# Performance work log

Hardware: AMD Instinct MI355X
Metric: run time of the kernel (lower is better)

## Reference

```python
import jax, jax.numpy as jnp
import numpy as np

B, H, N, D = 1, 8, 2048, 64  # n >> d: fastmax's intended long-seq / small-head-dim regime


def setup_inputs() -> dict:
    key = jax.random.key(0)
    kq, kk, kv, kr = jax.random.split(key, 4)
    q = jax.random.normal(kq, (B, H, N, D), dtype=jnp.float32)
    k = jax.random.normal(kk, (B, H, N, D), dtype=jnp.float32)
    v = jax.random.normal(kv, (B, H, N, D), dtype=jnp.float32)
    rpe_matrix = jax.random.normal(kr, (2 * N - 1, D), dtype=jnp.float32)
    return {"q": q, "k": k, "v": v, "rpe_matrix": rpe_matrix, "mask": 1}


def reference(q, k, v, rpe_matrix, mask):
    # Fastmax: 2nd-order Taylor approximation of softmax attention,
    # weight(i,j) = 1 + s_ij + s_ij^2 / 2 where s_ij = q_i . (k_j) + q_i . rpe[i-j+n-1],
    # normalized by the row-sum, optionally causal (mask).
    b, h, n, d = q.shape
    # content scores: (b,h,n,n)
    s = jnp.einsum('bhid,bhjd->bhij', q, k)
    # RPE scores: project q onto every relative-position embedding, then gather
    # the (i,j) -> i-j+n-1 diagonal structure.  qr: (b,h,n,2n-1)
    qr = jnp.einsum('bhid,md->bhim', q, rpe_matrix)
    i = jnp.arange(n)[:, None]
    j = jnp.arange(n)[None, :]
    rel = i - j + (n - 1)  # (n,n) in [0, 2n-2]
    s = s + jnp.take_along_axis(qr, rel[None, None], axis=-1)
    # Taylor-2 exp approximation
    w = 1.0 + s + 0.5 * s * s
    if mask:  # causal
        w = jnp.where(j <= i, w, 0.0)
    denom = jnp.sum(w, axis=-1, keepdims=True)  # (b,h,n,1)
    out = jnp.einsum('bhij,bhjd->bhid', w, v) / denom
    return out
```

## Files before the change

kernel.cpp:

```cpp
#include <hip/hip_runtime.h>
#include <hip/hip_bf16.h>

#define HH 8
#define NN 2048
#define DD 64

typedef __attribute__((ext_vector_type(8))) short bf16x8;
typedef __attribute__((ext_vector_type(4))) float f32x4;
typedef __attribute__((ext_vector_type(8))) unsigned short u16x8;
typedef unsigned short ushort_t;

static __device__ __forceinline__ unsigned short f2bf(float x) {
    union { float f; unsigned u; } un; un.f = x;
    unsigned r = un.u + 0x7FFFu + ((un.u >> 16) & 1u);
    return (unsigned short)(r >> 16);
}
static __device__ __forceinline__ unsigned short f2bf_t(float x) {
    union { float f; unsigned u; } un; un.f = x;
    return (unsigned short)(un.u >> 16);
}
static __device__ __forceinline__ float bf2f(unsigned short u) {
    union { unsigned u; float f; } un; un.u = ((unsigned)u) << 16;
    return un.f;
}

#define OFF_Q  0u
#define OFF_K  2097152u
#define OFF_VT 4194304u
#define OFF_R  6291456u
#define OFF_P  6815744u
#define WS_NEED 11272192u

#define NQ4 262144
#define NR4 65520
#define CVT_BLOCKS 2305
__global__ void pre_kernel(const float* __restrict__ q, const float* __restrict__ k,
                           const float* __restrict__ r, const float* __restrict__ v,
                           ushort_t* __restrict__ ws) {
    __shared__ __align__(16) ushort_t T[64][72];
    if (blockIdx.x < CVT_BLOCKS) {
        int idx = blockIdx.x * 256 + threadIdx.x;
        const float* src; ushort_t* dst; int off;
        if (idx < NQ4) { src = q; dst = (ushort_t*)((char*)ws + OFF_Q); off = idx; }
        else if (idx < 2 * NQ4) { src = k; dst = (ushort_t*)((char*)ws + OFF_K); off = idx - NQ4; }
        else if (idx < 2 * NQ4 + NR4) { src = r; dst = (ushort_t*)((char*)ws + OFF_R); off = idx - 2 * NQ4; }
        else return;
        float4 f = *(const float4*)&src[4 * (size_t)off];
        ushort4 u; u.x = f2bf(f.x); u.y = f2bf(f.y); u.z = f2bf(f.z); u.w = f2bf(f.w);
        *(ushort4*)&dst[4 * (size_t)off] = u;
    } else {
        ushort_t* vt = (ushort_t*)((char*)ws + OFF_VT);
        const int bb = blockIdx.x - CVT_BLOCKS;
        const int h = bb >> 5;
        const int n0 = (bb & 31) * 64;
        const int tid = threadIdx.x;
        const float* vh = v + (size_t)h * NN * DD;
        #pragma unroll
        for (int p = 0; p < 4; ++p) {
            int c = tid + 256 * p; int rr = c >> 4, dc = (c & 15) << 2;
            float4 f = *(const float4*)&vh[(size_t)(n0 + rr) * DD + dc];
            T[dc + 0][rr] = f2bf(f.x); T[dc + 1][rr] = f2bf(f.y);
            T[dc + 2][rr] = f2bf(f.z); T[dc + 3][rr] = f2bf(f.w);
        }
        __syncthreads();
        #pragma unroll
        for (int p = 0; p < 2; ++p) {
            int c = tid + 256 * p; int d = c >> 3, nn = (c & 7) << 3;
            *(u16x8*)&vt[((size_t)h * 64 + d) * NN + n0 + nn] = *(const u16x8*)&T[d][nn];
        }
    }
}

__global__ __launch_bounds__(256, 2)
void fastmax_main(const ushort_t* __restrict__ wsb, float* __restrict__ outg,
                  float* __restrict__ wsPart)
{
    __shared__ __align__(16) ushort_t Ks[2][64][72];
    __shared__ __align__(16) ushort_t Bs[2][96][72];
    __shared__ __align__(16) ushort_t Vts[2][64][72];
    __shared__ __align__(16) unsigned char U[12800];
    float* Epi = (float*)U;

    const ushort_t* qb  = (const ushort_t*)((const char*)wsb + OFF_Q);
    const ushort_t* kb  = (const ushort_t*)((const char*)wsb + OFF_K);
    const ushort_t* vtb = (const ushort_t*)((const char*)wsb + OFF_VT);
    const ushort_t* rb_ = (const ushort_t*)((const char*)wsb + OFF_R);

    const int tid = threadIdx.x;
    const int w   = tid >> 6;
    const int l   = tid & 63;
    const int lq  = l >> 4;
    const int ln  = l & 15;
    const int rt  = w & 1;
    const int ch  = w >> 1;

    ushort_t* tsW = (ushort_t*)(U + w * 1920);
    ushort_t* wsW = (ushort_t*)(U + 7680 + w * 1280);

    const int sb     = blockIdx.x & 1;
    const int stream = blockIdx.x >> 1;
    const int head   = stream & 7;
    const int p      = stream >> 3;
    const int tileA  = 63 - p;
    const int njtA   = (tileA >> 1) + 1;
    const int tileB  = p;
    const int njtB   = (tileB >> 1) + 1;

    const ushort_t* qh  = qb  + (size_t)head * NN * DD;
    const ushort_t* kh  = kb  + (size_t)head * NN * DD;
    const ushort_t* vth = vtb + (size_t)head * DD * NN;
    float*          oh  = outg + (size_t)head * NN * DD;

    const int sw = 16 * rt - 32 * ch + 32;

    u16x8 rk0, rk1, rbA, rbB, rbC, rv0, rv1;
    const int c0r = tid >> 3,         c0d = (tid & 7) << 3;
    const int c1r = (tid + 256) >> 3, c1d = ((tid + 256) & 7) << 3;
    const int c2r = (tid + 512) >> 3, c2d = ((tid + 512) & 7) << 3;

    #pragma unroll 1
    for (int tsel = 0; tsel < 2; ++tsel) {
        if (tsel == 1 && sb == 0) break;
        const int tile = tsel ? tileB : tileA;
        const int jlo  = tsel ? 0 : (sb ? 17 : 0);
        const int jhi  = tsel ? njtB : (sb ? njtA : 17);
        const int i0   = tile * 32;

        bf16x8 qf0 = *(const bf16x8*)&qh[(size_t)(i0 + 16 * rt + ln) * DD +  0 + 8 * lq];
        bf16x8 qf1 = *(const bf16x8*)&qh[(size_t)(i0 + 16 * rt + ln) * DD + 32 + 8 * lq];

        f32x4 acc0 = {0,0,0,0}, acc1 = {0,0,0,0}, acc2 = {0,0,0,0}, acc3 = {0,0,0,0};
        float denv0 = 0.f, denv1 = 0.f, denv2 = 0.f, denv3 = 0.f;

        {
            const int j0 = jlo * 64;
            const int relbase = i0 - j0 + 1984;
            rk0 = *(const u16x8*)&kh[(size_t)(j0 + c0r) * DD + c0d];
            rk1 = *(const u16x8*)&kh[(size_t)(j0 + c1r) * DD + c1d];
            int r0 = relbase + c0r; if (r0 > 4094) r0 = 4094;
            int r1 = relbase + c1r; if (r1 > 4094) r1 = 4094;
            int r2 = relbase + c2r; if (r2 > 4094) r2 = 4094;
            rbA = *(const u16x8*)&rb_[(size_t)r0 * DD + c0d];
            rbB = *(const u16x8*)&rb_[(size_t)r1 * DD + c1d];
            rbC = *(const u16x8*)&rb_[(size_t)r2 * DD + c2d];
            rv0 = *(const u16x8*)&vth[(size_t)c0r * NN + j0 + c0d];
            rv1 = *(const u16x8*)&vth[(size_t)c1r * NN + j0 + c1d];
        }

        int buf = 0;
        for (int jt = jlo; jt < jhi; ++jt) {
            const int j0 = jt * 64;

            *(u16x8*)&Ks[buf][c0r][c0d] = rk0;
            *(u16x8*)&Ks[buf][c1r][c1d] = rk1;
            *(u16x8*)&Bs[buf][c0r][c0d] = rbA;
            *(u16x8*)&Bs[buf][c1r][c1d] = rbB;
            *(u16x8*)&Bs[buf][c2r][c2d] = rbC;
            *(u16x8*)&Vts[buf][c0r][c0d] = rv0;
            *(u16x8*)&Vts[buf][c1r][c1d] = rv1;

            __syncthreads();

            if (jt + 1 < jhi) {
                const int jn = j0 + 64;
                const int relbase = i0 - jn + 1984;
                rk0 = *(const u16x8*)&kh[(size_t)(jn + c0r) * DD + c0d];
                rk1 = *(const u16x8*)&kh[(size_t)(jn + c1r) * DD + c1d];
                int r0 = relbase + c0r; if (r0 > 4094) r0 = 4094;
                int r1 = relbase + c1r; if (r1 > 4094) r1 = 4094;
                int r2 = relbase + c2r; if (r2 > 4094) r2 = 4094;
                rbA = *(const u16x8*)&rb_[(size_t)r0 * DD + c0d];
                rbB = *(const u16x8*)&rb_[(size_t)r1 * DD + c1d];
                rbC = *(const u16x8*)&rb_[(size_t)r2 * DD + c2d];
                rv0 = *(const u16x8*)&vth[(size_t)c0r * NN + jn + c0d];
                rv1 = *(const u16x8*)&vth[(size_t)c1r * NN + jn + c1d];
            }

            f32x4 s0 = {0,0,0,0}, s1 = {0,0,0,0};
            {
                bf16x8 b00 = *(const bf16x8*)&Ks[buf][32 * ch      + ln][ 0 + 8 * lq];
                bf16x8 b01 = *(const bf16x8*)&Ks[buf][32 * ch      + ln][32 + 8 * lq];
                bf16x8 b10 = *(const bf16x8*)&Ks[buf][32 * ch + 16 + ln][ 0 + 8 * lq];
                bf16x8 b11 = *(const bf16x8*)&Ks[buf][32 * ch + 16 + ln][32 + 8 * lq];
                s0 = __builtin_amdgcn_mfma_f32_16x16x32_bf16(qf0, b00, s0, 0, 0, 0);
                s0 = __builtin_amdgcn_mfma_f32_16x16x32_bf16(qf1, b01, s0, 0, 0, 0);
                s1 = __builtin_amdgcn_mfma_f32_16x16x32_bf16(qf0, b10, s1, 0, 0, 0);
                s1 = __builtin_amdgcn_mfma_f32_16x16x32_bf16(qf1, b11, s1, 0, 0, 0);
            }

            #pragma unroll
            for (int bt = 0; bt < 3; ++bt) {
                f32x4 t = {0,0,0,0};
                bf16x8 b0 = *(const bf16x8*)&Bs[buf][sw + 16 * bt + ln][ 0 + 8 * lq];
                bf16x8 b1 = *(const bf16x8*)&Bs[buf][sw + 16 * bt + ln][32 + 8 * lq];
                t = __builtin_amdgcn_mfma_f32_16x16x32_bf16(qf0, b0, t, 0, 0, 0);
                t = __builtin_amdgcn_mfma_f32_16x16x32_bf16(qf1, b1, t, 0, 0, 0);
                ushort4 pk;
                pk.x = f2bf_t(t[0]); pk.y = f2bf_t(t[1]);
                pk.z = f2bf_t(t[2]); pk.w = f2bf_t(t[3]);
                *(ushort4*)&tsW[(16 * bt + ln) * 20 + 4 * lq] = pk;
            }

            #pragma unroll
            for (int ct = 0; ct < 2; ++ct) {
                f32x4 sv = ct ? s1 : s0;
                #pragma unroll
                for (int e = 0; e < 4; ++e) {
                    int rp = 4 * lq + e;
                    int cp = 16 * ct + ln;
                    int bw = rp - cp + 31;
                    float s = sv[e] + bf2f(tsW[bw * 20 + rp]);
                    float wv = 1.0f + s + 0.5f * s * s;
                    if (j0 + 32 * ch + cp > i0 + 16 * rt + rp) wv = 0.0f;
                    union { float f; unsigned u; } uw; uw.f = wv;
                    wsW[rp * 40 + cp] = (ushort_t)(uw.u >> 16);
                    uw.u &= 0xffff0000u;
                    if (e == 0) denv0 += uw.f; else if (e == 1) denv1 += uw.f;
                    else if (e == 2) denv2 += uw.f; else denv3 += uw.f;
                }
            }

            {
                bf16x8 af = *(const bf16x8*)&wsW[ln * 40 + 8 * lq];
                bf16x8 b;
                b = *(const bf16x8*)&Vts[buf][ 0 + ln][32 * ch + 8 * lq];
                acc0 = __builtin_amdgcn_mfma_f32_16x16x32_bf16(af, b, acc0, 0, 0, 0);
                b = *(const bf16x8*)&Vts[buf][16 + ln][32 * ch + 8 * lq];
                acc1 = __builtin_amdgcn_mfma_f32_16x16x32_bf16(af, b, acc1, 0, 0, 0);
                b = *(const bf16x8*)&Vts[buf][32 + ln][32 * ch + 8 * lq];
                acc2 = __builtin_amdgcn_mfma_f32_16x16x32_bf16(af, b, acc2, 0, 0, 0);
                b = *(const bf16x8*)&Vts[buf][48 + ln][32 * ch + 8 * lq];
                acc3 = __builtin_amdgcn_mfma_f32_16x16x32_bf16(af, b, acc3, 0, 0, 0);
            }
            buf ^= 1;
        }

        #pragma unroll
        for (int off = 1; off <= 8; off <<= 1) {
            denv0 += __shfl_xor(denv0, off);
            denv1 += __shfl_xor(denv1, off);
            denv2 += __shfl_xor(denv2, off);
            denv3 += __shfl_xor(denv3, off);
        }

        __syncthreads();
        if (ch == 0) {
            #pragma unroll
            for (int e = 0; e < 4; ++e) {
                int r = 16 * rt + 4 * lq + e;
                Epi[r * 68 +  0 + ln] = acc0[e];
                Epi[r * 68 + 16 + ln] = acc1[e];
                Epi[r * 68 + 32 + ln] = acc2[e];
                Epi[r * 68 + 48 + ln] = acc3[e];
            }
            if (ln == 0) {
                Epi[(16 * rt + 4 * lq + 0) * 68 + 64] = denv0;
                Epi[(16 * rt + 4 * lq + 1) * 68 + 64] = denv1;
                Epi[(16 * rt + 4 * lq + 2) * 68 + 64] = denv2;
                Epi[(16 * rt + 4 * lq + 3) * 68 + 64] = denv3;
            }
        }
        __syncthreads();
        if (ch == 1) {
            #pragma unroll
            for (int e = 0; e < 4; ++e) {
                int r = 16 * rt + 4 * lq + e;
                Epi[r * 68 +  0 + ln] += acc0[e];
                Epi[r * 68 + 16 + ln] += acc1[e];
                Epi[r * 68 + 32 + ln] += acc2[e];
                Epi[r * 68 + 48 + ln] += acc3[e];
            }
            if (ln == 0) {
                Epi[(16 * rt + 4 * lq + 0) * 68 + 64] += denv0;
                Epi[(16 * rt + 4 * lq + 1) * 68 + 64] += denv1;
                Epi[(16 * rt + 4 * lq + 2) * 68 + 64] += denv2;
                Epi[(16 * rt + 4 * lq + 3) * 68 + 64] += denv3;
            }
        }
        __syncthreads();
        if (tsel == 0) {
            float* dst = wsPart + ((size_t)(head * 32 + p) * 2 + sb) * (32 * 68);
            for (int idx = tid; idx < 32 * 68; idx += 256) dst[idx] = Epi[idx];
        } else {
            #pragma unroll
            for (int e2 = 0; e2 < 8; ++e2) {
                int idx = tid + 256 * e2;
                int r = idx >> 6, d = idx & 63;
                oh[(size_t)(i0 + r) * DD + d] = Epi[r * 68 + d] / Epi[r * 68 + 64];
            }
        }
    }
}

__global__ void combine_kernel(const float* __restrict__ wsPart, float* __restrict__ outg) {
    const int blk = blockIdx.x;
    const int head = blk >> 5;
    const int p = blk & 31;
    const int tileA = 63 - p;
    const float* p0 = wsPart + (size_t)blk * 2 * (32 * 68);
    const float* p1 = p0 + 32 * 68;
    float* oh = outg + (size_t)head * NN * DD;
    #pragma unroll
    for (int e2 = 0; e2 < 8; ++e2) {
        int idx = threadIdx.x + 256 * e2;
        int r = idx >> 6, d = idx & 63;
        float num = p0[r * 68 + d] + p1[r * 68 + d];
        float den = p0[r * 68 + 64] + p1[r * 68 + 64];
        oh[(size_t)(tileA * 32 + r) * DD + d] = num / den;
    }
}

__global__ __launch_bounds__(256, 2)
void fastmax_fallback(const float* __restrict__ qg0, const float* __restrict__ kg0,
                      const float* __restrict__ vg0, const float* __restrict__ rg,
                      float* __restrict__ outg)
{
    __shared__ __align__(16) ushort_t Qs[32][72];
    __shared__ __align__(16) ushort_t Ks2[64][72];
    __shared__ __align__(16) ushort_t Bs2[96][72];
    __shared__ __align__(16) ushort_t Vts2[96][72];
    __shared__ __align__(16) float    Tsf[32][97];
    __shared__ __align__(16) ushort_t Wsf[32][72];
    __shared__ float denomLds[32];

    const int tid = threadIdx.x;
    const int w = tid >> 6, l = tid & 63, lq = l >> 4, ln = l & 15;
    const int head = blockIdx.x & 7, ib = blockIdx.x >> 3;
    const int it = 63 - ib, i0 = it * 32, njt = (it >> 1) + 1;
    const float* qg = qg0 + (size_t)head * NN * DD;
    const float* kg = kg0 + (size_t)head * NN * DD;
    const float* vg = vg0 + (size_t)head * NN * DD;
    float* og = outg + (size_t)head * NN * DD;
    {
        #pragma unroll
        for (int p = 0; p < 2; ++p) {
            int c = tid + 256 * p; int r = c >> 4, dc = (c & 15) << 2;
            float4 f = *(const float4*)&qg[(size_t)(i0 + r) * DD + dc];
            ushort4 u; u.x = f2bf(f.x); u.y = f2bf(f.y); u.z = f2bf(f.z); u.w = f2bf(f.w);
            *(ushort4*)&Qs[r][dc] = u;
        }
        for (int idx = tid; idx < 32 * 72; idx += 256) {
            int rr = idx / 72, cc = idx - rr * 72;
            Vts2[64 + rr][cc] = (rr == 0) ? (ushort_t)0x3F80 : (ushort_t)0;
        }
    }
    f32x4 a0 = {0,0,0,0}, a1 = {0,0,0,0}, a2 = {0,0,0,0};
    const int pr = w & 1, rt = w & 1, cp = w >> 1;
    for (int jt = 0; jt < njt; ++jt) {
        const int j0 = jt * 64;
        __syncthreads();
        #pragma unroll
        for (int p = 0; p < 4; ++p) {
            int c = tid + 256 * p; int r = c >> 4, dc = (c & 15) << 2;
            float4 f = *(const float4*)&kg[(size_t)(j0 + r) * DD + dc];
            ushort4 u; u.x = f2bf(f.x); u.y = f2bf(f.y); u.z = f2bf(f.z); u.w = f2bf(f.w);
            *(ushort4*)&Ks2[r][dc] = u;
        }
        const int relbase = i0 - j0 + 1984;
        #pragma unroll
        for (int p = 0; p < 6; ++p) {
            int c = tid + 256 * p; int r = c >> 4, dc = (c & 15) << 2;
            int row = relbase + r; if (row > 4094) row = 4094;
            float4 f = *(const float4*)&rg[(size_t)row * DD + dc];
            ushort4 u; u.x = f2bf(f.x); u.y = f2bf(f.y); u.z = f2bf(f.z); u.w = f2bf(f.w);
            *(ushort4*)&Bs2[r][dc] = u;
        }
        #pragma unroll
        for (int p = 0; p < 4; ++p) {
            int c = tid + 256 * p; int r = c >> 4, dc = (c & 15) << 2;
            float4 f = *(const float4*)&vg[(size_t)(j0 + r) * DD + dc];
            Vts2[dc + 0][r] = f2bf(f.x); Vts2[dc + 1][r] = f2bf(f.y);
            Vts2[dc + 2][r] = f2bf(f.z); Vts2[dc + 3][r] = f2bf(f.w);
        }
        __syncthreads();
        f32x4 s0 = {0,0,0,0}, s1 = {0,0,0,0};
        #pragma unroll
        for (int ks = 0; ks < 2; ++ks) {
            bf16x8 a = *(const bf16x8*)&Qs[16 * rt + ln][32 * ks + 8 * lq];
            bf16x8 b0 = *(const bf16x8*)&Ks2[32 * cp + ln][32 * ks + 8 * lq];
            bf16x8 b1 = *(const bf16x8*)&Ks2[32 * cp + 16 + ln][32 * ks + 8 * lq];
            s0 = __builtin_amdgcn_mfma_f32_16x16x32_bf16(a, b0, s0, 0, 0, 0);
            s1 = __builtin_amdgcn_mfma_f32_16x16x32_bf16(a, b1, s1, 0, 0, 0);
        }
        #pragma unroll
        for (int kk = 0; kk < 3; ++kk) {
            int bt = (w >> 1) + 2 * kk;
            f32x4 t = {0,0,0,0};
            #pragma unroll
            for (int ks = 0; ks < 2; ++ks) {
                bf16x8 a = *(const bf16x8*)&Qs[16 * rt + ln][32 * ks + 8 * lq];
                bf16x8 b = *(const bf16x8*)&Bs2[16 * bt + ln][32 * ks + 8 * lq];
                t = __builtin_amdgcn_mfma_f32_16x16x32_bf16(a, b, t, 0, 0, 0);
            }
            #pragma unroll
            for (int e = 0; e < 4; ++e) Tsf[16 * rt + 4 * lq + e][16 * bt + ln] = t[e];
        }
        __syncthreads();
        #pragma unroll
        for (int ct2 = 0; ct2 < 2; ++ct2) {
            f32x4 sv = ct2 ? s1 : s0;
            int c_loc = 32 * cp + 16 * ct2 + ln, j = j0 + c_loc;
            #pragma unroll
            for (int e = 0; e < 4; ++e) {
                int r_loc = 16 * rt + 4 * lq + e, i = i0 + r_loc;
                float s = sv[e] + Tsf[r_loc][r_loc - c_loc + 63];
                float wv = 1.0f + s + 0.5f * s * s;
                if (j > i) wv = 0.0f;
                Wsf[r_loc][c_loc] = f2bf(wv);
            }
        }
        __syncthreads();
        {
            bf16x8 af0 = *(const bf16x8*)&Wsf[16 * pr + ln][ 0 + 8 * lq];
            bf16x8 af1 = *(const bf16x8*)&Wsf[16 * pr + ln][32 + 8 * lq];
            int pn0 = w >> 1; bf16x8 b;
            b = *(const bf16x8*)&Vts2[16 * (pn0 + 0) + ln][ 0 + 8 * lq];
            a0 = __builtin_amdgcn_mfma_f32_16x16x32_bf16(af0, b, a0, 0, 0, 0);
            b = *(const bf16x8*)&Vts2[16 * (pn0 + 0) + ln][32 + 8 * lq];
            a0 = __builtin_amdgcn_mfma_f32_16x16x32_bf16(af1, b, a0, 0, 0, 0);
            b = *(const bf16x8*)&Vts2[16 * (pn0 + 2) + ln][ 0 + 8 * lq];
            a1 = __builtin_amdgcn_mfma_f32_16x16x32_bf16(af0, b, a1, 0, 0, 0);
            b = *(const bf16x8*)&Vts2[16 * (pn0 + 2) + ln][32 + 8 * lq];
            a1 = __builtin_amdgcn_mfma_f32_16x16x32_bf16(af1, b, a1, 0, 0, 0);
            b = *(const bf16x8*)&Vts2[16 * (pn0 + 4) + ln][ 0 + 8 * lq];
            a2 = __builtin_amdgcn_mfma_f32_16x16x32_bf16(af0, b, a2, 0, 0, 0);
            b = *(const bf16x8*)&Vts2[16 * (pn0 + 4) + ln][32 + 8 * lq];
            a2 = __builtin_amdgcn_mfma_f32_16x16x32_bf16(af1, b, a2, 0, 0, 0);
        }
    }
    if (w < 2 && ln == 0) {
        #pragma unroll
        for (int e = 0; e < 4; ++e) denomLds[16 * pr + 4 * lq + e] = a2[e];
    }
    __syncthreads();
    #pragma unroll
    for (int k = 0; k < 2; ++k) {
        int pn = (w >> 1) + 2 * k;
        f32x4 acc = k ? a1 : a0;
        #pragma unroll
        for (int e = 0; e < 4; ++e) {
            int r_loc = 16 * pr + 4 * lq + e;
            og[(size_t)(i0 + r_loc) * DD + 16 * pn + ln] = acc[e] / denomLds[r_loc];
        }
    }
}

extern "C" void kernel_launch(void* const* d_in, const int* in_sizes, int n_in,
                              void* d_out, int out_size, void* d_ws, size_t ws_size,
                              hipStream_t stream) {
    const float* q   = (const float*)d_in[0];
    const float* k   = (const float*)d_in[1];
    const float* v   = (const float*)d_in[2];
    const float* rpe = (const float*)d_in[3];
    float* out = (float*)d_out;

    if (ws_size >= WS_NEED) {
        ushort_t* wsb = (ushort_t*)d_ws;
        float* wsPart = (float*)((char*)d_ws + OFF_P);
        hipLaunchKernelGGL(pre_kernel, dim3(CVT_BLOCKS + 256), dim3(256), 0, stream,
                           q, k, rpe, v, wsb);
        hipLaunchKernelGGL(fastmax_main, dim3(512), dim3(256), 0, stream,
                           wsb, out, wsPart);
        hipLaunchKernelGGL(combine_kernel, dim3(256), dim3(256), 0, stream, wsPart, out);
    } else {
        hipLaunchKernelGGL(fastmax_fallback, dim3(512), dim3(256), 0, stream,
                           q, k, v, rpe, out);
    }
}
```

Before: 103.5 us.

## Fuse split-tile combine into main kernel via atomic arrival flags

Drops the separate combine kernel. Each split-tile block writes its partial sums, fences, and atomically bumps a per-tile counter; the second block to arrive reads its partner's partial and writes the normalized output. The pre-kernel zeroes the flags. The per-iteration barrier is also moved after the next-tile global prefetch loads are issued. This saves one kernel launch and a pass over the partials, at the cost of fence and atomic overhead and a reliance on correct memory ordering.

```diff
diff --git a/kernel.cpp b/kernel.cpp
--- a/kernel.cpp
+++ b/kernel.cpp
@@ -29,7 +29,8 @@
 #define OFF_VT 4194304u
 #define OFF_R  6291456u
 #define OFF_P  6815744u
-#define WS_NEED 11272192u
+#define OFF_F  11272192u
+#define WS_NEED 11273216u
 
 #define NQ4 262144
 #define NR4 65520
@@ -38,6 +39,8 @@
                            const float* __restrict__ r, const float* __restrict__ v,
                            ushort_t* __restrict__ ws) {
     __shared__ __align__(16) ushort_t T[64][72];
+    if (blockIdx.x == CVT_BLOCKS && threadIdx.x < 256)
+        ((int*)((char*)ws + OFF_F))[threadIdx.x] = 0;
     if (blockIdx.x < CVT_BLOCKS) {
         int idx = blockIdx.x * 256 + threadIdx.x;
         const float* src; ushort_t* dst; int off;
@@ -73,12 +76,13 @@
 
 __global__ __launch_bounds__(256, 2)
 void fastmax_main(const ushort_t* __restrict__ wsb, float* __restrict__ outg,
-                  float* __restrict__ wsPart)
+                  float* __restrict__ wsPart, int* __restrict__ flags)
 {
     __shared__ __align__(16) ushort_t Ks[2][64][72];
     __shared__ __align__(16) ushort_t Bs[2][96][72];
     __shared__ __align__(16) ushort_t Vts[2][64][72];
     __shared__ __align__(16) unsigned char U[12800];
+    __shared__ int flagOld;
     float* Epi = (float*)U;
 
     const ushort_t* qb  = (const ushort_t*)((const char*)wsb + OFF_Q);
@@ -159,8 +163,6 @@
             *(u16x8*)&Vts[buf][c0r][c0d] = rv0;
             *(u16x8*)&Vts[buf][c1r][c1d] = rv1;
 
-            __syncthreads();
-
             if (jt + 1 < jhi) {
                 const int jn = j0 + 64;
                 const int relbase = i0 - jn + 1984;
@@ -175,6 +177,8 @@
                 rv0 = *(const u16x8*)&vth[(size_t)c0r * NN + jn + c0d];
                 rv1 = *(const u16x8*)&vth[(size_t)c1r * NN + jn + c1d];
             }
+
+            __syncthreads();
 
             f32x4 s0 = {0,0,0,0}, s1 = {0,0,0,0};
             {
@@ -281,6 +285,22 @@
         if (tsel == 0) {
             float* dst = wsPart + ((size_t)(head * 32 + p) * 2 + sb) * (32 * 68);
             for (int idx = tid; idx < 32 * 68; idx += 256) dst[idx] = Epi[idx];
+            __threadfence();
+            __syncthreads();
+            if (tid == 0) flagOld = atomicAdd(&flags[head * 32 + p], 1);
+            __syncthreads();
+            if (flagOld == 1) {
+                __threadfence();
+                const float* pp = wsPart + ((size_t)(head * 32 + p) * 2 + (sb ^ 1)) * (32 * 68);
+                #pragma unroll
+                for (int e2 = 0; e2 < 8; ++e2) {
+                    int idx = tid + 256 * e2;
+                    int r = idx >> 6, d = idx & 63;
+                    float num = Epi[r * 68 + d] + pp[r * 68 + d];
+                    float den = Epi[r * 68 + 64] + pp[r * 68 + 64];
+                    oh[(size_t)(i0 + r) * DD + d] = num / den;
+                }
+            }
         } else {
             #pragma unroll
             for (int e2 = 0; e2 < 8; ++e2) {
@@ -289,24 +309,6 @@
                 oh[(size_t)(i0 + r) * DD + d] = Epi[r * 68 + d] / Epi[r * 68 + 64];
             }
         }
-    }
-}
-
-__global__ void combine_kernel(const float* __restrict__ wsPart, float* __restrict__ outg) {
-    const int blk = blockIdx.x;
-    const int head = blk >> 5;
-    const int p = blk & 31;
-    const int tileA = 63 - p;
-    const float* p0 = wsPart + (size_t)blk * 2 * (32 * 68);
-    const float* p1 = p0 + 32 * 68;
-    float* oh = outg + (size_t)head * NN * DD;
-    #pragma unroll
-    for (int e2 = 0; e2 < 8; ++e2) {
-        int idx = threadIdx.x + 256 * e2;
-        int r = idx >> 6, d = idx & 63;
-        float num = p0[r * 68 + d] + p1[r * 68 + d];
-        float den = p0[r * 68 + 64] + p1[r * 68 + 64];
-        oh[(size_t)(tileA * 32 + r) * DD + d] = num / den;
     }
 }
 
@@ -457,11 +459,11 @@
     if (ws_size >= WS_NEED) {
         ushort_t* wsb = (ushort_t*)d_ws;
         float* wsPart = (float*)((char*)d_ws + OFF_P);
+        int* flags = (int*)((char*)d_ws + OFF_F);
         hipLaunchKernelGGL(pre_kernel, dim3(CVT_BLOCKS + 256), dim3(256), 0, stream,
                            q, k, rpe, v, wsb);
         hipLaunchKernelGGL(fastmax_main, dim3(512), dim3(256), 0, stream,
-                           wsb, out, wsPart);
-        hipLaunchKernelGGL(combine_kernel, dim3(256), dim3(256), 0, stream, wsPart, out);
+                           wsb, out, wsPart, flags);
     } else {
         hipLaunchKernelGGL(fastmax_fallback, dim3(512), dim3(256), 0, stream,
                            q, k, v, rpe, out);
```

After: 166.7 us. 61.0% more time.
